# Kernel tuning notes

Measured on AMD Instinct MI355X. Metric: run time of the kernel, lower is better.

Reference implementation:

```python
import jax, jax.numpy as jnp
import numpy as np

B, C, R, E = 8192, 32, 24, 128
NUM_LOC = 100000
NUM_INNER = 200000   # inner_node_embed has NUM_INNER+1 rows; row 0 is padding_idx
NUM_SLICES = 24


def setup_inputs() -> dict:
    key = jax.random.key(0)
    ks = jax.random.split(key, 7)
    context = jax.random.randint(ks[0], (B, C), 0, NUM_LOC)
    route = jax.random.randint(ks[1], (B, R), 0, NUM_INNER + 1)
    lr = jax.random.randint(ks[2], (B, R), 0, 2)
    slice_idx = jax.random.randint(ks[3], (B,), 0, NUM_SLICES)
    input_embed = jax.random.normal(ks[4], (NUM_LOC, E), dtype=jnp.float32)
    inner_node_embed = jax.random.normal(ks[5], (NUM_INNER + 1, E), dtype=jnp.float32).at[0].set(0.0)
    slice_node_embed = jax.random.uniform(ks[6], (NUM_SLICES, E), dtype=jnp.float32)
    return {
        "context": context, "route": route, "lr": lr, "slice_idx": slice_idx,
        "input_embed": input_embed, "inner_node_embed": inner_node_embed,
        "slice_node_embed": slice_node_embed,
    }


def reference(context, route, lr, slice_idx, input_embed, inner_node_embed, slice_node_embed):
    # context embedding: gather + sum over context window -> (B, E)
    ctx = input_embed[context].sum(axis=1)
    # slice prediction: (B, num_slices) softmax, gather target slice prob -> (B,)
    slice_logits = jnp.einsum('se,be->bs', slice_node_embed, ctx)
    slice_prob = jax.nn.softmax(slice_logits, axis=1)
    slice_pre = jnp.take_along_axis(slice_prob, slice_idx[:, None], axis=1)[:, 0]
    # route scores: (B, R)
    dot = jnp.einsum('bre,be->br', inner_node_embed[route], ctx)
    lr_pre = jax.nn.sigmoid(dot)
    # (2p)^lr - p  -> p if lr==1, (1-p) if lr==0
    route_hidden = jnp.power(2.0 * lr_pre, lr.astype(lr_pre.dtype)) - lr_pre
    # padded route positions (route id == 0) contribute factor 1
    route_hidden = jnp.where(route == 0, jnp.ones((), lr_pre.dtype), route_hidden)
    # per-level product loop collapsed into a single prod over route dim
    pr_route = slice_pre * jnp.prod(route_hidden, axis=1)
    return 1.0 - pr_route.mean()
```

## Files before the change

kernel.cpp:

```cpp
#include <hip/hip_runtime.h>

#define BATCH    8192
#define CTX      32
#define ROUTES   24
#define EDIM     128
#define NSLICE   24
#define WPB      4
#define NBLOCKS  (BATCH / WPB)

__global__ __launch_bounds__(256, 8) void tale_fused(
    const int* __restrict__ context,
    const int* __restrict__ route,
    const int* __restrict__ lr,
    const int* __restrict__ slice_idx,
    const float* __restrict__ input_embed,
    const float* __restrict__ inner_node_embed,
    const float* __restrict__ slice_node_embed,
    float* __restrict__ out)
{
    const int tid  = threadIdx.x;
    const int lane = tid & 63;
    const int half = lane >> 5;
    const int sub  = lane & 31;
    const int w    = tid >> 6;
    const int b    = blockIdx.x * WPB + w;

    __shared__ float bs[WPB];

    int cidx = 0, ridx = 0, lridx = 0;
    if (lane < CTX) cidx = context[b * CTX + lane];
    if (lane < ROUTES) {
        ridx  = route[b * ROUTES + lane];
        lridx = lr[b * ROUTES + lane];
    }
    const int si = slice_idx[b];

    float4 acc = make_float4(0.f, 0.f, 0.f, 0.f);
    #pragma unroll
    for (int i = 0; i < 16; ++i) {
        const int idx = __shfl(cidx, i + (half << 4));
        const float4 v = *reinterpret_cast<const float4*>(
            input_embed + (size_t)idx * EDIM + (sub << 2));
        acc.x += v.x; acc.y += v.y; acc.z += v.z; acc.w += v.w;
    }
    acc.x += __shfl_xor(acc.x, 32);
    acc.y += __shfl_xor(acc.y, 32);
    acc.z += __shfl_xor(acc.z, 32);
    acc.w += __shfl_xor(acc.w, 32);

    float prodv = 1.f;
    #pragma unroll
    for (int i = 0; i < 12; ++i) {
        const int d   = 2 * i + half;
        const int idx = __shfl(ridx, d);
        const int l   = __shfl(lridx, d);
        const float4 v = *reinterpret_cast<const float4*>(
            inner_node_embed + (size_t)idx * EDIM + (sub << 2));
        float p = v.x * acc.x + v.y * acc.y + v.z * acc.z + v.w * acc.w;
        p += __shfl_xor(p, 16);
        p += __shfl_xor(p, 8);
        p += __shfl_xor(p, 4);
        p += __shfl_xor(p, 2);
        p += __shfl_xor(p, 1);
        const float sg = 1.f / (1.f + __expf(-p));
        float h = l ? sg : (1.f - sg);
        if (idx == 0) h = 1.f;
        prodv *= h;
    }
    prodv *= __shfl_xor(prodv, 32);

    float m = -3.0e38f, den = 0.f, selv = 0.f;
    #pragma unroll
    for (int i = 0; i < 12; ++i) {
        const int s = 2 * i + half;
        const float4 v = *reinterpret_cast<const float4*>(
            slice_node_embed + s * EDIM + (sub << 2));
        float p = v.x * acc.x + v.y * acc.y + v.z * acc.z + v.w * acc.w;
        p += __shfl_xor(p, 16);
        p += __shfl_xor(p, 8);
        p += __shfl_xor(p, 4);
        p += __shfl_xor(p, 2);
        p += __shfl_xor(p, 1);
        const float mN = fmaxf(m, p);
        den = den * __expf(m - mN) + __expf(p - mN);
        m = mN;
        if (s == si) selv = p;
    }
    const float m_o   = __shfl_xor(m, 32);
    const float den_o = __shfl_xor(den, 32);
    const float M     = fmaxf(m, m_o);
    const float dtot  = den * __expf(m - M) + den_o * __expf(m_o - M);
    const float sel   = __shfl(selv, (si & 1) << 5);
    const float slice_pre = __expf(sel - M) / dtot;

    const float pr = slice_pre * prodv;

    if (lane == 0) bs[w] = pr;
    __syncthreads();
    if (tid == 0) {
        const float s = bs[0] + bs[1] + bs[2] + bs[3];
        atomicAdd(out, 1.0f / NBLOCKS - s * (1.0f / BATCH));
    }
}

extern "C" void kernel_launch(void* const* d_in, const int* in_sizes, int n_in,
                              void* d_out, int out_size, void* d_ws, size_t ws_size,
                              hipStream_t stream)
{
    const int*   context          = (const int*)  d_in[0];
    const int*   route            = (const int*)  d_in[1];
    const int*   lr               = (const int*)  d_in[2];
    const int*   slice_idx        = (const int*)  d_in[3];
    const float* input_embed      = (const float*)d_in[4];
    const float* inner_node_embed = (const float*)d_in[5];
    const float* slice_node_embed = (const float*)d_in[6];
    float* out = (float*)d_out;

    hipMemsetAsync(out, 0, sizeof(float), stream);

    tale_fused<<<NBLOCKS, 64 * WPB, 0, stream>>>(
        context, route, lr, slice_idx,
        input_embed, inner_node_embed, slice_node_embed, out);
}
```

Measured before the change: 207.1 us.

## Batch gather loads and interleave route and slice dot products

Context rows are now gathered in groups of eight loads issued before any accumulation, which raises memory-level parallelism. Route and slice dot products are fused into one loop that issues four route and four slice loads per batch and interleaves their shuffle reductions. The online softmax is replaced by a max-then-sum pass over stored logits. The occupancy hint in launch bounds is lowered from 8 to 5 to leave room for the extra registers, so fewer waves may be resident.

```diff
diff --git a/kernel.cpp b/kernel.cpp
--- a/kernel.cpp
+++ b/kernel.cpp
@@ -8,7 +8,7 @@
 #define WPB      4
 #define NBLOCKS  (BATCH / WPB)
 
-__global__ __launch_bounds__(256, 8) void tale_fused(
+__global__ __launch_bounds__(256, 5) void tale_fused(
     const int* __restrict__ context,
     const int* __restrict__ route,
     const int* __restrict__ lr,
@@ -37,11 +37,19 @@
 
     float4 acc = make_float4(0.f, 0.f, 0.f, 0.f);
     #pragma unroll
-    for (int i = 0; i < 16; ++i) {
-        const int idx = __shfl(cidx, i + (half << 4));
-        const float4 v = *reinterpret_cast<const float4*>(
-            input_embed + (size_t)idx * EDIM + (sub << 2));
-        acc.x += v.x; acc.y += v.y; acc.z += v.z; acc.w += v.w;
+    for (int g = 0; g < 2; ++g) {
+        float4 pv[8];
+        #pragma unroll
+        for (int j = 0; j < 8; ++j) {
+            const int idx = __shfl(cidx, (half << 4) + g * 8 + j);
+            pv[j] = *reinterpret_cast<const float4*>(
+                input_embed + (size_t)idx * EDIM + (sub << 2));
+        }
+        #pragma unroll
+        for (int j = 0; j < 8; ++j) {
+            acc.x += pv[j].x; acc.y += pv[j].y;
+            acc.z += pv[j].z; acc.w += pv[j].w;
+        }
     }
     acc.x += __shfl_xor(acc.x, 32);
     acc.y += __shfl_xor(acc.y, 32);
@@ -49,49 +57,64 @@
     acc.w += __shfl_xor(acc.w, 32);
 
     float prodv = 1.f;
+    float sd[12];
+    float selv = 0.f;
     #pragma unroll
-    for (int i = 0; i < 12; ++i) {
-        const int d   = 2 * i + half;
-        const int idx = __shfl(ridx, d);
-        const int l   = __shfl(lridx, d);
-        const float4 v = *reinterpret_cast<const float4*>(
-            inner_node_embed + (size_t)idx * EDIM + (sub << 2));
-        float p = v.x * acc.x + v.y * acc.y + v.z * acc.z + v.w * acc.w;
-        p += __shfl_xor(p, 16);
-        p += __shfl_xor(p, 8);
-        p += __shfl_xor(p, 4);
-        p += __shfl_xor(p, 2);
-        p += __shfl_xor(p, 1);
-        const float sg = 1.f / (1.f + __expf(-p));
-        float h = l ? sg : (1.f - sg);
-        if (idx == 0) h = 1.f;
-        prodv *= h;
+    for (int bat = 0; bat < 3; ++bat) {
+        float4 rv[4], sv[4];
+        #pragma unroll
+        for (int j = 0; j < 4; ++j) {
+            const int i   = bat * 4 + j;
+            const int d   = 2 * i + half;
+            const int idx = __shfl(ridx, d);
+            rv[j] = *reinterpret_cast<const float4*>(
+                inner_node_embed + (size_t)idx * EDIM + (sub << 2));
+            sv[j] = *reinterpret_cast<const float4*>(
+                slice_node_embed + d * EDIM + (sub << 2));
+        }
+        float rp[4], sp[4];
+        #pragma unroll
+        for (int j = 0; j < 4; ++j) {
+            rp[j] = rv[j].x * acc.x + rv[j].y * acc.y
+                  + rv[j].z * acc.z + rv[j].w * acc.w;
+            sp[j] = sv[j].x * acc.x + sv[j].y * acc.y
+                  + sv[j].z * acc.z + sv[j].w * acc.w;
+        }
+        #pragma unroll
+        for (int off = 16; off > 0; off >>= 1) {
+            #pragma unroll
+            for (int j = 0; j < 4; ++j) {
+                rp[j] += __shfl_xor(rp[j], off);
+                sp[j] += __shfl_xor(sp[j], off);
+            }
+        }
+        #pragma unroll
+        for (int j = 0; j < 4; ++j) {
+            const int i   = bat * 4 + j;
+            const int d   = 2 * i + half;
+            const int idx = __shfl(ridx, d);
+            const int l   = __shfl(lridx, d);
+            const float sg = 1.f / (1.f + __expf(-rp[j]));
+            float h = l ? sg : (1.f - sg);
+            if (idx == 0) h = 1.f;
+            prodv *= h;
+            sd[i] = sp[j];
+            if (d == si) selv = sp[j];
+        }
     }
     prodv *= __shfl_xor(prodv, 32);
 
-    float m = -3.0e38f, den = 0.f, selv = 0.f;
+    float m01 = fmaxf(sd[0], sd[1]),  m23 = fmaxf(sd[2], sd[3]);
+    float m45 = fmaxf(sd[4], sd[5]),  m67 = fmaxf(sd[6], sd[7]);
+    float m89 = fmaxf(sd[8], sd[9]),  mAB = fmaxf(sd[10], sd[11]);
+    float mh = fmaxf(fmaxf(fmaxf(m01, m23), fmaxf(m45, m67)), fmaxf(m89, mAB));
+    const float M = fmaxf(mh, __shfl_xor(mh, 32));
+    float den = 0.f;
     #pragma unroll
-    for (int i = 0; i < 12; ++i) {
-        const int s = 2 * i + half;
-        const float4 v = *reinterpret_cast<const float4*>(
-            slice_node_embed + s * EDIM + (sub << 2));
-        float p = v.x * acc.x + v.y * acc.y + v.z * acc.z + v.w * acc.w;
-        p += __shfl_xor(p, 16);
-        p += __shfl_xor(p, 8);
-        p += __shfl_xor(p, 4);
-        p += __shfl_xor(p, 2);
-        p += __shfl_xor(p, 1);
-        const float mN = fmaxf(m, p);
-        den = den * __expf(m - mN) + __expf(p - mN);
-        m = mN;
-        if (s == si) selv = p;
-    }
-    const float m_o   = __shfl_xor(m, 32);
-    const float den_o = __shfl_xor(den, 32);
-    const float M     = fmaxf(m, m_o);
-    const float dtot  = den * __expf(m - M) + den_o * __expf(m_o - M);
-    const float sel   = __shfl(selv, (si & 1) << 5);
-    const float slice_pre = __expf(sel - M) / dtot;
+    for (int i = 0; i < 12; ++i) den += __expf(sd[i] - M);
+    den += __shfl_xor(den, 32);
+    const float sel = __shfl(selv, (si & 1) << 5);
+    const float slice_pre = __expf(sel - M) / den;
 
     const float pr = slice_pre * prodv;
 
```

After: 211.7 us. 1.02x slower.

## Split context gather into separate kernel and batch route-row loads up front

Applied to the files above, without the earlier changes.

The fused kernel becomes two kernels. The first gathers and sums the context embeddings into a workspace buffer, with 32 threads per batch row. The second reads that buffer, issues all 12 route-embedding loads before any compute, and replaces the online softmax with a two-pass max-then-sum. The aim is more memory-level parallelism and shorter dependency chains on the random gathers, paid for by an extra launch and a round trip of the context sums through global memory, and occupancy is lowered to 4 blocks per CU in the second kernel.

```diff
diff --git a/kernel.cpp b/kernel.cpp
--- a/kernel.cpp
+++ b/kernel.cpp
@@ -6,14 +6,37 @@
 #define EDIM     128
 #define NSLICE   24
 #define WPB      4
-#define NBLOCKS  (BATCH / WPB)
+#define K2_BLOCKS (BATCH / WPB)
 
-__global__ __launch_bounds__(256, 8) void tale_fused(
+__global__ __launch_bounds__(256) void tale_ctx(
     const int* __restrict__ context,
+    const float* __restrict__ input_embed,
+    float* __restrict__ ctx_out)
+{
+    const int gid  = blockIdx.x * 256 + threadIdx.x;
+    const int lane = threadIdx.x & 63;
+    const int half = lane >> 5;
+    const int sub  = lane & 31;
+    const int b    = gid >> 5;
+
+    const int cidx = context[b * CTX + sub];
+
+    float4 acc = make_float4(0.f, 0.f, 0.f, 0.f);
+    #pragma unroll
+    for (int c = 0; c < CTX; ++c) {
+        const int idx = __shfl(cidx, (half << 5) + c);
+        const float4 v = *reinterpret_cast<const float4*>(
+            input_embed + (size_t)idx * EDIM + (sub << 2));
+        acc.x += v.x; acc.y += v.y; acc.z += v.z; acc.w += v.w;
+    }
+    *reinterpret_cast<float4*>(ctx_out + (size_t)b * EDIM + (sub << 2)) = acc;
+}
+
+__global__ __launch_bounds__(256, 4) void tale_dots(
     const int* __restrict__ route,
     const int* __restrict__ lr,
     const int* __restrict__ slice_idx,
-    const float* __restrict__ input_embed,
+    const float* __restrict__ ctx_in,
     const float* __restrict__ inner_node_embed,
     const float* __restrict__ slice_node_embed,
     float* __restrict__ out)
@@ -27,71 +50,69 @@
 
     __shared__ float bs[WPB];
 
-    int cidx = 0, ridx = 0, lridx = 0;
-    if (lane < CTX) cidx = context[b * CTX + lane];
+    int ridx = 0, lridx = 0;
     if (lane < ROUTES) {
         ridx  = route[b * ROUTES + lane];
         lridx = lr[b * ROUTES + lane];
     }
     const int si = slice_idx[b];
 
-    float4 acc = make_float4(0.f, 0.f, 0.f, 0.f);
-    #pragma unroll
-    for (int i = 0; i < 16; ++i) {
-        const int idx = __shfl(cidx, i + (half << 4));
-        const float4 v = *reinterpret_cast<const float4*>(
-            input_embed + (size_t)idx * EDIM + (sub << 2));
-        acc.x += v.x; acc.y += v.y; acc.z += v.z; acc.w += v.w;
-    }
-    acc.x += __shfl_xor(acc.x, 32);
-    acc.y += __shfl_xor(acc.y, 32);
-    acc.z += __shfl_xor(acc.z, 32);
-    acc.w += __shfl_xor(acc.w, 32);
+    const float4 acc = *reinterpret_cast<const float4*>(
+        ctx_in + (size_t)b * EDIM + (sub << 2));
 
-    float prodv = 1.f;
+    int   idxs[12];
+    float4 rv[12];
     #pragma unroll
     for (int i = 0; i < 12; ++i) {
-        const int d   = 2 * i + half;
-        const int idx = __shfl(ridx, d);
-        const int l   = __shfl(lridx, d);
+        idxs[i] = __shfl(ridx, 2 * i + half);
+        rv[i] = *reinterpret_cast<const float4*>(
+            inner_node_embed + (size_t)idxs[i] * EDIM + (sub << 2));
+    }
+
+    float sd[12], selv = 0.f;
+    #pragma unroll
+    for (int i = 0; i < 12; ++i) {
+        const int d = 2 * i + half;
         const float4 v = *reinterpret_cast<const float4*>(
-            inner_node_embed + (size_t)idx * EDIM + (sub << 2));
+            slice_node_embed + d * EDIM + (sub << 2));
         float p = v.x * acc.x + v.y * acc.y + v.z * acc.z + v.w * acc.w;
         p += __shfl_xor(p, 16);
         p += __shfl_xor(p, 8);
         p += __shfl_xor(p, 4);
         p += __shfl_xor(p, 2);
         p += __shfl_xor(p, 1);
-        const float sg = 1.f / (1.f + __expf(-p));
-        float h = l ? sg : (1.f - sg);
-        if (idx == 0) h = 1.f;
-        prodv *= h;
+        sd[i] = p;
+        if (d == si) selv = p;
     }
-    prodv *= __shfl_xor(prodv, 32);
+    float m01 = fmaxf(sd[0], sd[1]),  m23 = fmaxf(sd[2], sd[3]);
+    float m45 = fmaxf(sd[4], sd[5]),  m67 = fmaxf(sd[6], sd[7]);
+    float m89 = fmaxf(sd[8], sd[9]),  mAB = fmaxf(sd[10], sd[11]);
+    float mh = fmaxf(fmaxf(fmaxf(m01, m23), fmaxf(m45, m67)), fmaxf(m89, mAB));
+    const float M = fmaxf(mh, __shfl_xor(mh, 32));
+    float den = 0.f;
+    #pragma unroll
+    for (int i = 0; i < 12; ++i) den += __expf(sd[i] - M);
+    den += __shfl_xor(den, 32);
+    const float sel = __shfl(selv, (si & 1) << 5);
+    const float slice_pre = __expf(sel - M) / den;
 
-    float m = -3.0e38f, den = 0.f, selv = 0.f;
+    float prodv = 1.f;
     #pragma unroll
     for (int i = 0; i < 12; ++i) {
-        const int s = 2 * i + half;
-        const float4 v = *reinterpret_cast<const float4*>(
-            slice_node_embed + s * EDIM + (sub << 2));
-        float p = v.x * acc.x + v.y * acc.y + v.z * acc.z + v.w * acc.w;
+        float p = rv[i].x * acc.x + rv[i].y * acc.y
+                + rv[i].z * acc.z + rv[i].w * acc.w;
         p += __shfl_xor(p, 16);
         p += __shfl_xor(p, 8);
         p += __shfl_xor(p, 4);
         p += __shfl_xor(p, 2);
         p += __shfl_xor(p, 1);
-        const float mN = fmaxf(m, p);
-        den = den * __expf(m - mN) + __expf(p - mN);
-        m = mN;
-        if (s == si) selv = p;
+        const int l = __shfl(lridx, 2 * i + half);
+        const float sg = 1.f / (1.f + __expf(-p));
+        float h = l ? sg : (1.f - sg);
+        if (idxs[i] == 0) h = 1.f;
+        prodv *= h;
     }
-    const float m_o   = __shfl_xor(m, 32);
-    const float den_o = __shfl_xor(den, 32);
-    const float M     = fmaxf(m, m_o);
-    const float dtot  = den * __expf(m - M) + den_o * __expf(m_o - M);
-    const float sel   = __shfl(selv, (si & 1) << 5);
-    const float slice_pre = __expf(sel - M) / dtot;
+    prodv *= __shfl_xor(prodv, 32);
 
     const float pr = slice_pre * prodv;
 
@@ -99,7 +120,7 @@
     __syncthreads();
     if (tid == 0) {
         const float s = bs[0] + bs[1] + bs[2] + bs[3];
-        atomicAdd(out, 1.0f / NBLOCKS - s * (1.0f / BATCH));
+        atomicAdd(out, 1.0f / K2_BLOCKS - s * (1.0f / BATCH));
     }
 }
 
@@ -115,10 +136,12 @@
     const float* inner_node_embed = (const float*)d_in[5];
     const float* slice_node_embed = (const float*)d_in[6];
     float* out = (float*)d_out;
+    float* ctx = (float*)d_ws;
 
     hipMemsetAsync(out, 0, sizeof(float), stream);
 
-    tale_fused<<<NBLOCKS, 64 * WPB, 0, stream>>>(
-        context, route, lr, slice_idx,
-        input_embed, inner_node_embed, slice_node_embed, out);
+    tale_ctx<<<BATCH * 32 / 256, 256, 0, stream>>>(context, input_embed, ctx);
+
+    tale_dots<<<K2_BLOCKS, 64 * WPB, 0, stream>>>(
+        route, lr, slice_idx, ctx, inner_node_embed, slice_node_embed, out);
 }
```

Result: slower. 215.1 us (+3.9%).
